# Performance work log

Measured on AMD Instinct MI355X. Metric: run time of the kernel, lower is better.

The kernel has to match this reference:

```python
import jax, jax.numpy as jnp
import numpy as np

B, L, H, NF = 8192, 2048, 2048, 8  # batch, latent, h_last_dim, n_flows


def setup_inputs() -> dict:
    key = jax.random.key(0)
    k0, k1, k2, k3 = jax.random.split(key, 4)
    scale = 0.02  # keep v well-conditioned through repeated linears
    return {
        "z": jax.random.normal(k0, (B, L), jnp.float32),
        "h_last": jax.random.normal(k1, (B, H), jnp.float32),
        "W0": jax.random.normal(k2, (L, H), jnp.float32) * scale,
        "b0": jnp.zeros((L,), jnp.float32),
        "Ws": jax.random.normal(k3, (NF - 1, L, L), jnp.float32) * scale,
        "bs": jnp.zeros((NF - 1, L), jnp.float32),
    }


def _hflow(v, z):
    # z_new = z - 2 * v (v . z) / ||v||^2  (Householder reflection, O(L) form of
    # the original's explicit vv^T bmm)
    vz = jnp.sum(v * z, axis=1, keepdims=True)       # [B,1]
    norm_sq = jnp.sum(v * v, axis=1, keepdims=True)  # [B,1]
    return z - 2.0 * v * (vz / norm_sq)


def reference(z, h_last, W0, b0, Ws, bs):
    # first v from h_last, then chain: v_{j+1} = Linear(v_j), z_{j+1} = HF(v_{j+1}, z_j)
    v = h_last @ W0.T + b0
    z = _hflow(v, z)

    def step(carry, wb):
        v, z = carry
        W, b = wb
        v = v @ W.T + b
        z = _hflow(v, z)
        return (v, z), None

    (v, z), _ = jax.lax.scan(step, (v, z), (Ws, bs))
    return z
```

## Files before the change

kernel.cpp:

```cpp
#include <hip/hip_runtime.h>
#include <hip/hip_bf16.h>
#include <stdint.h>

#define B_  8192
#define L_  2048
#define NF_ 8

typedef __bf16 bf16_t;
typedef __bf16 bf16x8 __attribute__((ext_vector_type(8)));
typedef __bf16 bf16x4 __attribute__((ext_vector_type(4)));
typedef float  floatx4 __attribute__((ext_vector_type(4)));

__device__ __forceinline__ bf16_t f2bf(float f) {
    union { float f; uint32_t u; } a; a.f = f;
    uint32_t r = a.u + 0x7fffu + ((a.u >> 16) & 1u);
    union { uint16_t s; bf16_t b; } o; o.s = (uint16_t)(r >> 16);
    return o.b;
}

#define GLD16(gp, lp)                                                          \
    __builtin_amdgcn_global_load_lds(                                          \
        (const __attribute__((address_space(1))) void*)(gp),                   \
        (__attribute__((address_space(3))) void*)(lp), 16, 0, 0)

__global__ __launch_bounds__(256) void cvt_kernel(const float* __restrict__ s,
                                                  bf16_t* __restrict__ d) {
    const int i = blockIdx.x * 256 + threadIdx.x;
    float4 f = ((const float4*)s)[i];
    bf16x4 o = { f2bf(f.x), f2bf(f.y), f2bf(f.z), f2bf(f.w) };
    ((bf16x4*)d)[i] = o;
}

__global__ __launch_bounds__(256, 4) void gemm_bt_kernel(
    const bf16_t* __restrict__ A,
    const bf16_t* __restrict__ W,
    const float*  __restrict__ bias,
    bf16_t* __restrict__ Vb)
{
    constexpr int K = L_;
    constexpr int N = L_;
    __shared__ alignas(16) bf16_t sA[128 * 64];
    __shared__ alignas(16) bf16_t sB[128 * 64];

    const int tid  = threadIdx.x;
    const int lane = tid & 63;
    const int wave = tid >> 6;
    const int wm   = wave >> 1;
    const int wn   = wave & 1;
    const int tm   = blockIdx.y * 128;
    const int tn   = blockIdx.x * 128;

    const int srow = tid >> 3;
    const int schk = (tid & 7) ^ (srow & 7);
    const bf16_t* Ag = A + (size_t)(tm + srow) * K + schk * 8;
    const bf16_t* Wg = W + (size_t)(tn + srow) * K + schk * 8;
    bf16_t* sAp = sA + tid * 8;
    bf16_t* sBp = sB + tid * 8;

    floatx4 acc[4][4] = {};

    const int ra = wm * 64 + (lane & 15);
    const int rb = wn * 64 + (lane & 15);
    const int q  = lane >> 4;
    const int rx = lane & 7;

    for (int kt = 0; kt < K; kt += 64) {
#pragma unroll
        for (int i = 0; i < 4; ++i) {
            GLD16(Ag + kt + (size_t)(32 * i) * K, sAp + i * 2048);
            GLD16(Wg + kt + (size_t)(32 * i) * K, sBp + i * 2048);
        }
        asm volatile("s_waitcnt vmcnt(0)" ::: "memory");
        __syncthreads();

#pragma unroll
        for (int ks = 0; ks < 2; ++ks) {
            const int c = ks * 4 + q;
            const int pc = (c ^ rx) * 8;
            bf16x8 af[4], bw[4];
#pragma unroll
            for (int i = 0; i < 4; ++i) {
                af[i] = *(const bf16x8*)(sA + (ra + i * 16) * 64 + pc);
                bw[i] = *(const bf16x8*)(sB + (rb + i * 16) * 64 + pc);
            }
#pragma unroll
            for (int mi = 0; mi < 4; ++mi)
#pragma unroll
                for (int ni = 0; ni < 4; ++ni)
                    acc[mi][ni] = __builtin_amdgcn_mfma_f32_16x16x32_bf16(
                        af[mi], bw[ni], acc[mi][ni], 0, 0, 0);
        }
        __syncthreads();
    }

    const int row0 = tm + wm * 64 + (lane >> 4) * 4;
    const int col0 = tn + wn * 64 + (lane & 15);
#pragma unroll
    for (int ni = 0; ni < 4; ++ni) {
        const int col = col0 + ni * 16;
        const float bv = bias[col];
#pragma unroll
        for (int mi = 0; mi < 4; ++mi) {
#pragma unroll
            for (int r = 0; r < 4; ++r) {
                Vb[(size_t)(row0 + mi * 16 + r) * N + col] = f2bf(acc[mi][ni][r] + bv);
            }
        }
    }
}

__global__ __launch_bounds__(256, 4) void hflow_kernel(
    const bf16_t* __restrict__ V, const float* __restrict__ zin,
    float* __restrict__ zout)
{
    const int lane = threadIdx.x & 63;
    const int row  = blockIdx.x * 4 + (threadIdx.x >> 6);
    const bf16x8* v8 = (const bf16x8*)(V + (size_t)row * L_);
    const float4* z4 = (const float4*)(zin + (size_t)row * L_);
    float4*       zo = (float4*)(zout + (size_t)row * L_);

    bf16x8 v[4];
    float4 z[8];
#pragma unroll
    for (int j = 0; j < 4; ++j) {
        const int idx = lane + 64 * j;
        v[j]         = v8[idx];
        z[2 * j]     = z4[2 * idx];
        z[2 * j + 1] = z4[2 * idx + 1];
    }

    float vf[32];
#pragma unroll
    for (int j = 0; j < 4; ++j)
#pragma unroll
        for (int e = 0; e < 8; ++e) vf[j * 8 + e] = (float)v[j][e];

    float vz = 0.f, vv = 0.f;
#pragma unroll
    for (int j = 0; j < 4; ++j) {
        const float* f = vf + j * 8;
        vz += f[0] * z[2*j].x + f[1] * z[2*j].y + f[2] * z[2*j].z + f[3] * z[2*j].w
            + f[4] * z[2*j+1].x + f[5] * z[2*j+1].y + f[6] * z[2*j+1].z + f[7] * z[2*j+1].w;
        vv += f[0]*f[0] + f[1]*f[1] + f[2]*f[2] + f[3]*f[3]
            + f[4]*f[4] + f[5]*f[5] + f[6]*f[6] + f[7]*f[7];
    }

#pragma unroll
    for (int off = 1; off < 64; off <<= 1) {
        vz += __shfl_xor(vz, off);
        vv += __shfl_xor(vv, off);
    }
    const float s = 2.0f * vz / vv;

#pragma unroll
    for (int j = 0; j < 4; ++j) {
        const int idx = lane + 64 * j;
        const float* f = vf + j * 8;
        float4 a = z[2*j], b = z[2*j+1];
        a.x -= s * f[0]; a.y -= s * f[1]; a.z -= s * f[2]; a.w -= s * f[3];
        b.x -= s * f[4]; b.y -= s * f[5]; b.z -= s * f[6]; b.w -= s * f[7];
        zo[2 * idx]     = a;
        zo[2 * idx + 1] = b;
    }
}

extern "C" void kernel_launch(void* const* d_in, const int* in_sizes, int n_in,
                              void* d_out, int out_size, void* d_ws, size_t ws_size,
                              hipStream_t stream) {
    (void)in_sizes; (void)n_in; (void)out_size; (void)ws_size;
    const float* z_in   = (const float*)d_in[0];
    const float* h_last = (const float*)d_in[1];
    const float* W0     = (const float*)d_in[2];
    const float* b0     = (const float*)d_in[3];
    const float* Wsp    = (const float*)d_in[4];
    const float* bsp    = (const float*)d_in[5];
    float* z_out = (float*)d_out;

    char* ws = (char*)d_ws;
    bf16_t* Wbf = (bf16_t*)ws;
    bf16_t* Vp0 = (bf16_t*)(ws + (size_t)NF_ * L_ * L_ * 2);
    bf16_t* Vp1 = Vp0 + (size_t)B_ * L_;

    cvt_kernel<<<(L_ * L_) / 1024, 256, 0, stream>>>(W0, Wbf);
    cvt_kernel<<<((NF_ - 1) * L_ * L_) / 1024, 256, 0, stream>>>(
        Wsp, Wbf + (size_t)L_ * L_);
    cvt_kernel<<<(B_ * L_) / 1024, 256, 0, stream>>>(h_last, Vp0);

    dim3 ggrid(L_ / 128, B_ / 128);
    bf16_t* bufs[2] = { Vp0, Vp1 };
    for (int j = 0; j < NF_; ++j) {
        const float* bias = (j == 0) ? b0 : bsp + (size_t)(j - 1) * L_;
        const bf16_t* Wj = Wbf + (size_t)j * L_ * L_;
        bf16_t* Ain = bufs[j & 1];
        bf16_t* Vout = bufs[(j + 1) & 1];
        gemm_bt_kernel<<<ggrid, 256, 0, stream>>>(Ain, Wj, bias, Vout);
        hflow_kernel<<<B_ / 4, 256, 0, stream>>>(
            Vout, (j == 0) ? z_in : z_out, z_out);
    }
}
```

Measured before the change: 1.019 ms.

## Rewrite GEMM as 256x256 tile with 4-stage LDS pipeline and 8 waves

The bf16 GEMM moves from 128x128 tiles with single-buffered K=64 steps and a full vmcnt(0) wait, to 256x256 tiles with 512 threads, K=32 steps and a four-deep LDS ring. Global-to-LDS loads run three tiles ahead, and the MFMA phases are interleaved with barriers and setprio. The aim is to hide global load latency and raise arithmetic intensity per block. In exchange the kernel uses 128KB of LDS and more accumulator registers, and the grid shrinks to 256 blocks, which may leave CUs underused.

```diff
diff --git a/kernel.cpp b/kernel.cpp
--- a/kernel.cpp
+++ b/kernel.cpp
@@ -31,76 +31,120 @@
     ((bf16x4*)d)[i] = o;
 }
 
-__global__ __launch_bounds__(256, 4) void gemm_bt_kernel(
+#define VM8  asm volatile("s_waitcnt vmcnt(8)" ::: "memory")
+#define VM4  asm volatile("s_waitcnt vmcnt(4)" ::: "memory")
+#define VM0  asm volatile("s_waitcnt vmcnt(0)" ::: "memory")
+#define VMX  do {} while (0)
+
+__global__ __launch_bounds__(512, 2) void gemm_bt_kernel(
     const bf16_t* __restrict__ A,
     const bf16_t* __restrict__ W,
     const float*  __restrict__ bias,
     bf16_t* __restrict__ Vb)
 {
-    constexpr int K = L_;
-    constexpr int N = L_;
-    __shared__ alignas(16) bf16_t sA[128 * 64];
-    __shared__ alignas(16) bf16_t sB[128 * 64];
+    constexpr int K  = L_;
+    constexpr int N  = L_;
+    constexpr int NT = K / 32;
+    __shared__ alignas(16) bf16_t lds[4][16384];
 
     const int tid  = threadIdx.x;
     const int lane = tid & 63;
     const int wave = tid >> 6;
-    const int wm   = wave >> 1;
-    const int wn   = wave & 1;
-    const int tm   = blockIdx.y * 128;
-    const int tn   = blockIdx.x * 128;
-
-    const int srow = tid >> 3;
-    const int schk = (tid & 7) ^ (srow & 7);
-    const bf16_t* Ag = A + (size_t)(tm + srow) * K + schk * 8;
-    const bf16_t* Wg = W + (size_t)(tn + srow) * K + schk * 8;
-    bf16_t* sAp = sA + tid * 8;
-    bf16_t* sBp = sB + tid * 8;
-
-    floatx4 acc[4][4] = {};
-
-    const int ra = wm * 64 + (lane & 15);
-    const int rb = wn * 64 + (lane & 15);
-    const int q  = lane >> 4;
-    const int rx = lane & 7;
-
-    for (int kt = 0; kt < K; kt += 64) {
-#pragma unroll
-        for (int i = 0; i < 4; ++i) {
-            GLD16(Ag + kt + (size_t)(32 * i) * K, sAp + i * 2048);
-            GLD16(Wg + kt + (size_t)(32 * i) * K, sBp + i * 2048);
-        }
-        asm volatile("s_waitcnt vmcnt(0)" ::: "memory");
-        __syncthreads();
-
-#pragma unroll
-        for (int ks = 0; ks < 2; ++ks) {
-            const int c = ks * 4 + q;
-            const int pc = (c ^ rx) * 8;
-            bf16x8 af[4], bw[4];
-#pragma unroll
-            for (int i = 0; i < 4; ++i) {
-                af[i] = *(const bf16x8*)(sA + (ra + i * 16) * 64 + pc);
-                bw[i] = *(const bf16x8*)(sB + (rb + i * 16) * 64 + pc);
-            }
-#pragma unroll
-            for (int mi = 0; mi < 4; ++mi)
-#pragma unroll
-                for (int ni = 0; ni < 4; ++ni)
-                    acc[mi][ni] = __builtin_amdgcn_mfma_f32_16x16x32_bf16(
-                        af[mi], bw[ni], acc[mi][ni], 0, 0, 0);
-        }
-        __syncthreads();
-    }
-
-    const int row0 = tm + wm * 64 + (lane >> 4) * 4;
-    const int col0 = tn + wn * 64 + (lane & 15);
+    const int wm   = wave >> 2;
+    const int wn   = wave & 3;
+    const int tm   = blockIdx.y * 256;
+    const int tn   = blockIdx.x * 256;
+
+    const int r0 = tid >> 2;
+    const int lc = (tid & 3) ^ ((tid >> 3) & 3);
+    const bf16_t* Ag = A + (size_t)(tm + r0) * K + lc * 8;
+    const bf16_t* Wg = W + (size_t)(tn + r0) * K + lc * 8;
+    const int dA = tid * 8;
+    const int dB = 8192 + tid * 8;
+
+    const int l15 = lane & 15;
+    const int pq  = (((lane >> 4) ^ ((lane >> 1) & 3))) * 8;
+    const int aOff = (wm * 128 + l15) * 32 + pq;
+    const int bOff = 8192 + (wn * 64 + l15) * 32 + pq;
+
+    floatx4 acc[8][4] = {};
+
+    auto stageA = [&](int u) {
+        bf16_t* d = &lds[u & 3][dA];
+        const bf16_t* g = Ag + u * 32;
+        GLD16(g, d);
+        GLD16(g + (size_t)128 * K, d + 4096);
+    };
+    auto stageB = [&](int u) {
+        bf16_t* d = &lds[u & 3][dB];
+        const bf16_t* g = Wg + u * 32;
+        GLD16(g, d);
+        GLD16(g + (size_t)128 * K, d + 4096);
+    };
+
+    stageA(0); stageB(0);
+    stageA(1); stageB(1);
+    stageA(2); stageB(2);
+    VM8;
+    asm volatile("s_barrier" ::: "memory");
+
+#define TILE_BODY(T, STG, VMCB)                                                \
+    {                                                                          \
+        const int t_ = (T);                                                    \
+        const bf16_t* sl = &lds[t_ & 3][0];                                    \
+        bf16x8 af[4], bw[4];                                                   \
+                                                \
+        if (STG) stageA(t_ + 3);                                               \
+        _Pragma("unroll")                                                      \
+        for (int mi = 0; mi < 4; ++mi)                                         \
+            af[mi] = *(const bf16x8*)(sl + aOff + mi * 512);                   \
+        _Pragma("unroll")                                                      \
+        for (int ni = 0; ni < 4; ++ni)                                         \
+            bw[ni] = *(const bf16x8*)(sl + bOff + ni * 512);                   \
+        asm volatile("s_barrier" ::: "memory");                                \
+        __builtin_amdgcn_sched_barrier(0);                                     \
+        __builtin_amdgcn_s_setprio(1);                                         \
+        _Pragma("unroll")                                                      \
+        for (int mi = 0; mi < 4; ++mi)                                         \
+            _Pragma("unroll")                                                  \
+            for (int ni = 0; ni < 4; ++ni)                                     \
+                acc[mi][ni] = __builtin_amdgcn_mfma_f32_16x16x32_bf16(         \
+                    af[mi], bw[ni], acc[mi][ni], 0, 0, 0);                     \
+        __builtin_amdgcn_s_setprio(0);                                         \
+        asm volatile("s_barrier" ::: "memory");                                \
+                     \
+        if (STG) stageB(t_ + 3);                                               \
+        _Pragma("unroll")                                                      \
+        for (int mi = 0; mi < 4; ++mi)                                         \
+            af[mi] = *(const bf16x8*)(sl + aOff + (mi + 4) * 512);             \
+        asm volatile("s_barrier" ::: "memory");                                \
+        __builtin_amdgcn_sched_barrier(0);                                     \
+        __builtin_amdgcn_s_setprio(1);                                         \
+        _Pragma("unroll")                                                      \
+        for (int mi = 0; mi < 4; ++mi)                                         \
+            _Pragma("unroll")                                                  \
+            for (int ni = 0; ni < 4; ++ni)                                     \
+                acc[mi + 4][ni] = __builtin_amdgcn_mfma_f32_16x16x32_bf16(     \
+                    af[mi], bw[ni], acc[mi + 4][ni], 0, 0, 0);                 \
+        __builtin_amdgcn_s_setprio(0);                                         \
+        VMCB;                                                                  \
+        asm volatile("s_barrier" ::: "memory");                                \
+    }
+
+    for (int t = 0; t < NT - 3; ++t) TILE_BODY(t, 1, VM8);
+    TILE_BODY(NT - 3, 0, VM4);
+    TILE_BODY(NT - 2, 0, VM0);
+    TILE_BODY(NT - 1, 0, VMX);
+#undef TILE_BODY
+
+    const int row0 = tm + wm * 128 + (lane >> 4) * 4;
+    const int col0 = tn + wn * 64 + l15;
 #pragma unroll
     for (int ni = 0; ni < 4; ++ni) {
         const int col = col0 + ni * 16;
         const float bv = bias[col];
 #pragma unroll
-        for (int mi = 0; mi < 4; ++mi) {
+        for (int mi = 0; mi < 8; ++mi) {
 #pragma unroll
             for (int r = 0; r < 4; ++r) {
                 Vb[(size_t)(row0 + mi * 16 + r) * N + col] = f2bf(acc[mi][ni][r] + bv);
@@ -186,14 +230,14 @@
         Wsp, Wbf + (size_t)L_ * L_);
     cvt_kernel<<<(B_ * L_) / 1024, 256, 0, stream>>>(h_last, Vp0);
 
-    dim3 ggrid(L_ / 128, B_ / 128);
+    dim3 ggrid(L_ / 256, B_ / 256);
     bf16_t* bufs[2] = { Vp0, Vp1 };
     for (int j = 0; j < NF_; ++j) {
         const float* bias = (j == 0) ? b0 : bsp + (size_t)(j - 1) * L_;
         const bf16_t* Wj = Wbf + (size_t)j * L_ * L_;
         bf16_t* Ain = bufs[j & 1];
         bf16_t* Vout = bufs[(j + 1) & 1];
-        gemm_bt_kernel<<<ggrid, 256, 0, stream>>>(Ain, Wj, bias, Vout);
+        gemm_bt_kernel<<<ggrid, 512, 0, stream>>>(Ain, Wj, bias, Vout);
         hflow_kernel<<<B_ / 4, 256, 0, stream>>>(
             Vout, (j == 0) ? z_in : z_out, z_out);
     }
```

Measured after the change: 1.125 ms. +10.5%, slower.

## Store all flow v's and apply Householder reflections in one fused pass

Applied to the files above, without the earlier changes.

Each GEMM output v_j is now kept in its own workspace slice, and a single kernel applies all eight Householder reflections per row while keeping z in registers, prefetching the next v. This removes the repeated fp32 z read/write (8x B*L*4 bytes each way) and seven kernel launches. The cost is a much larger workspace (NF extra bf16 V buffers) and writing and re-reading every v. The old per-step path is kept as a fallback when the workspace is too small.

```diff
diff --git a/kernel.cpp b/kernel.cpp
--- a/kernel.cpp
+++ b/kernel.cpp
@@ -109,65 +109,87 @@
     }
 }
 
-__global__ __launch_bounds__(256, 4) void hflow_kernel(
-    const bf16_t* __restrict__ V, const float* __restrict__ zin,
-    float* __restrict__ zout)
+__global__ __launch_bounds__(256) void hflowN_kernel(
+    const bf16_t* __restrict__ Vall,
+    int nf,
+    const float* __restrict__ zin, float* __restrict__ zout)
 {
     const int lane = threadIdx.x & 63;
     const int row  = blockIdx.x * 4 + (threadIdx.x >> 6);
-    const bf16x8* v8 = (const bf16x8*)(V + (size_t)row * L_);
     const float4* z4 = (const float4*)(zin + (size_t)row * L_);
     float4*       zo = (float4*)(zout + (size_t)row * L_);
 
-    bf16x8 v[4];
     float4 z[8];
 #pragma unroll
     for (int j = 0; j < 4; ++j) {
         const int idx = lane + 64 * j;
-        v[j]         = v8[idx];
         z[2 * j]     = z4[2 * idx];
         z[2 * j + 1] = z4[2 * idx + 1];
     }
 
-    float vf[32];
-#pragma unroll
-    for (int j = 0; j < 4; ++j)
-#pragma unroll
-        for (int e = 0; e < 8; ++e) vf[j * 8 + e] = (float)v[j][e];
-
-    float vz = 0.f, vv = 0.f;
-#pragma unroll
-    for (int j = 0; j < 4; ++j) {
-        const float* f = vf + j * 8;
-        vz += f[0] * z[2*j].x + f[1] * z[2*j].y + f[2] * z[2*j].z + f[3] * z[2*j].w
-            + f[4] * z[2*j+1].x + f[5] * z[2*j+1].y + f[6] * z[2*j+1].z + f[7] * z[2*j+1].w;
-        vv += f[0]*f[0] + f[1]*f[1] + f[2]*f[2] + f[3]*f[3]
-            + f[4]*f[4] + f[5]*f[5] + f[6]*f[6] + f[7]*f[7];
-    }
-
-#pragma unroll
-    for (int off = 1; off < 64; off <<= 1) {
-        vz += __shfl_xor(vz, off);
-        vv += __shfl_xor(vv, off);
-    }
-    const float s = 2.0f * vz / vv;
+    const size_t vstride = (size_t)B_ * L_;
+    const bf16x8* v8 = (const bf16x8*)(Vall + (size_t)row * L_);
+
+    bf16x8 vcur[4];
+#pragma unroll
+    for (int j = 0; j < 4; ++j) vcur[j] = v8[lane + 64 * j];
+
+    for (int f = 0; f < nf; ++f) {
+        bf16x8 vnxt[4];
+        if (f + 1 < nf) {
+            const bf16x8* vn = (const bf16x8*)((const bf16_t*)v8 + (size_t)(f + 1) * vstride);
+#pragma unroll
+            for (int j = 0; j < 4; ++j) vnxt[j] = vn[lane + 64 * j];
+        }
+
+        float vf[32];
+#pragma unroll
+        for (int j = 0; j < 4; ++j)
+#pragma unroll
+            for (int e = 0; e < 8; ++e) vf[j * 8 + e] = (float)vcur[j][e];
+
+        float vz = 0.f, vv = 0.f;
+#pragma unroll
+        for (int j = 0; j < 4; ++j) {
+            const float* fp = vf + j * 8;
+            vz += fp[0] * z[2*j].x + fp[1] * z[2*j].y + fp[2] * z[2*j].z + fp[3] * z[2*j].w
+                + fp[4] * z[2*j+1].x + fp[5] * z[2*j+1].y + fp[6] * z[2*j+1].z + fp[7] * z[2*j+1].w;
+            vv += fp[0]*fp[0] + fp[1]*fp[1] + fp[2]*fp[2] + fp[3]*fp[3]
+                + fp[4]*fp[4] + fp[5]*fp[5] + fp[6]*fp[6] + fp[7]*fp[7];
+        }
+
+#pragma unroll
+        for (int off = 1; off < 64; off <<= 1) {
+            vz += __shfl_xor(vz, off);
+            vv += __shfl_xor(vv, off);
+        }
+        const float s = 2.0f * vz / vv;
+
+#pragma unroll
+        for (int j = 0; j < 4; ++j) {
+            const float* fp = vf + j * 8;
+            z[2*j].x -= s * fp[0]; z[2*j].y -= s * fp[1];
+            z[2*j].z -= s * fp[2]; z[2*j].w -= s * fp[3];
+            z[2*j+1].x -= s * fp[4]; z[2*j+1].y -= s * fp[5];
+            z[2*j+1].z -= s * fp[6]; z[2*j+1].w -= s * fp[7];
+        }
+
+#pragma unroll
+        for (int j = 0; j < 4; ++j) vcur[j] = vnxt[j];
+    }
 
 #pragma unroll
     for (int j = 0; j < 4; ++j) {
         const int idx = lane + 64 * j;
-        const float* f = vf + j * 8;
-        float4 a = z[2*j], b = z[2*j+1];
-        a.x -= s * f[0]; a.y -= s * f[1]; a.z -= s * f[2]; a.w -= s * f[3];
-        b.x -= s * f[4]; b.y -= s * f[5]; b.z -= s * f[6]; b.w -= s * f[7];
-        zo[2 * idx]     = a;
-        zo[2 * idx + 1] = b;
+        zo[2 * idx]     = z[2 * j];
+        zo[2 * idx + 1] = z[2 * j + 1];
     }
 }
 
 extern "C" void kernel_launch(void* const* d_in, const int* in_sizes, int n_in,
                               void* d_out, int out_size, void* d_ws, size_t ws_size,
                               hipStream_t stream) {
-    (void)in_sizes; (void)n_in; (void)out_size; (void)ws_size;
+    (void)in_sizes; (void)n_in; (void)out_size;
     const float* z_in   = (const float*)d_in[0];
     const float* h_last = (const float*)d_in[1];
     const float* W0     = (const float*)d_in[2];
@@ -177,24 +199,43 @@
     float* z_out = (float*)d_out;
 
     char* ws = (char*)d_ws;
+    const size_t wbytes = (size_t)NF_ * L_ * L_ * 2;
+    const size_t vbytes = (size_t)B_ * L_ * 2;
+
     bf16_t* Wbf = (bf16_t*)ws;
-    bf16_t* Vp0 = (bf16_t*)(ws + (size_t)NF_ * L_ * L_ * 2);
-    bf16_t* Vp1 = Vp0 + (size_t)B_ * L_;
-
     cvt_kernel<<<(L_ * L_) / 1024, 256, 0, stream>>>(W0, Wbf);
     cvt_kernel<<<((NF_ - 1) * L_ * L_) / 1024, 256, 0, stream>>>(
         Wsp, Wbf + (size_t)L_ * L_);
-    cvt_kernel<<<(B_ * L_) / 1024, 256, 0, stream>>>(h_last, Vp0);
 
     dim3 ggrid(L_ / 128, B_ / 128);
-    bf16_t* bufs[2] = { Vp0, Vp1 };
-    for (int j = 0; j < NF_; ++j) {
-        const float* bias = (j == 0) ? b0 : bsp + (size_t)(j - 1) * L_;
-        const bf16_t* Wj = Wbf + (size_t)j * L_ * L_;
-        bf16_t* Ain = bufs[j & 1];
-        bf16_t* Vout = bufs[(j + 1) & 1];
-        gemm_bt_kernel<<<ggrid, 256, 0, stream>>>(Ain, Wj, bias, Vout);
-        hflow_kernel<<<B_ / 4, 256, 0, stream>>>(
-            Vout, (j == 0) ? z_in : z_out, z_out);
-    }
-}
+
+    if (ws_size >= wbytes + vbytes + (size_t)NF_ * vbytes) {
+        bf16_t* Hbf  = (bf16_t*)(ws + wbytes);
+        bf16_t* Vall = Hbf + (size_t)B_ * L_;
+        cvt_kernel<<<(B_ * L_) / 1024, 256, 0, stream>>>(h_last, Hbf);
+
+        for (int j = 0; j < NF_; ++j) {
+            const float* bias = (j == 0) ? b0 : bsp + (size_t)(j - 1) * L_;
+            const bf16_t* Wj = Wbf + (size_t)j * L_ * L_;
+            const bf16_t* Ain = (j == 0) ? Hbf : Vall + (size_t)(j - 1) * B_ * L_;
+            bf16_t* Vout = Vall + (size_t)j * B_ * L_;
+            gemm_bt_kernel<<<ggrid, 256, 0, stream>>>(Ain, Wj, bias, Vout);
+        }
+        hflowN_kernel<<<B_ / 4, 256, 0, stream>>>(Vall, NF_, z_in, z_out);
+    } else {
+        bf16_t* Vp0 = (bf16_t*)(ws + wbytes);
+        bf16_t* Vp1 = Vp0 + (size_t)B_ * L_;
+        cvt_kernel<<<(B_ * L_) / 1024, 256, 0, stream>>>(h_last, Vp0);
+
+        bf16_t* bufs[2] = { Vp0, Vp1 };
+        for (int j = 0; j < NF_; ++j) {
+            const float* bias = (j == 0) ? b0 : bsp + (size_t)(j - 1) * L_;
+            const bf16_t* Wj = Wbf + (size_t)j * L_ * L_;
+            bf16_t* Ain = bufs[j & 1];
+            bf16_t* Vout = bufs[(j + 1) & 1];
+            gemm_bt_kernel<<<ggrid, 256, 0, stream>>>(Ain, Wj, bias, Vout);
+            hflowN_kernel<<<B_ / 4, 256, 0, stream>>>(
+                Vout, 1, (j == 0) ? z_in : z_out, z_out);
+        }
+    }
+}
```

Result: faster. 889.1 us (-12.7%).
